# Kernel optimization log

Hardware: AMD Instinct MI355X
Metric: run time of the kernel (lower is better)

## Reference

```python
import jax, jax.numpy as jnp
import numpy as np

EPS = 1e-10   # eps added inside cumprod, as in _compute_weights
FAR = 1e10    # last delta, as in forward()
NEAR_D, FAR_D = 2.0, 6.0  # typical NeRF near/far bounds for depth sampling

N_RAYS, N_PTS = 65536, 128


def setup_inputs() -> dict:
    key = jax.random.key(0)
    k1, k2, k3 = jax.random.split(key, 3)
    # densities are non-negative (raw sigma output after relu/softplus)
    density = jax.random.uniform(k1, (N_RAYS, N_PTS), dtype=jnp.float32) * 2.0
    feature = jax.random.uniform(k2, (N_RAYS, N_PTS, 3), dtype=jnp.float32)
    # monotonically increasing sample depths along each ray in [NEAR_D, FAR_D]
    depth_values = jnp.sort(
        jax.random.uniform(k3, (N_RAYS, N_PTS), dtype=jnp.float32,
                           minval=NEAR_D, maxval=FAR_D), axis=-1)
    return {"density": density, "feature": feature, "depth_values": depth_values}


def reference(density, feature, depth_values):
    # deltas: diff of sample depths, last delta = 1e10  -> [N, P]
    deltas = jnp.concatenate(
        [depth_values[..., 1:] - depth_values[..., :-1],
         jnp.full_like(depth_values[..., :1], FAR)], axis=-1)
    alpha = 1.0 - jnp.exp(-deltas * density)                      # [N, P]
    # transmittance: cumprod(1-alpha+eps) rolled right with T[...,0]=1
    Tinc = jnp.cumprod(1.0 - alpha + EPS, axis=-1)                # [N, P]
    T = jnp.concatenate([jnp.ones_like(Tinc[..., :1]), Tinc[..., :-1]], axis=-1)
    weights = T * alpha                                           # [N, P]
    # weighted feature (rgb) and depth aggregation over samples
    rgb = jnp.einsum('np,npc->nc', weights, feature)              # [N, 3]
    depth = jnp.einsum('np,npc->nc', weights,
                       jnp.broadcast_to(depth_values[..., None], feature.shape))  # [N, 3]
    return rgb, depth
```

## Files before the change

### kernel.cpp

```cpp
#include <hip/hip_runtime.h>

#define N_PTS 128
#define EPS_F 1e-10f
#define FAR_F 1e10f
#define MAX_GRID 2048

template<int CTRL, int ROW_MASK>
__device__ __forceinline__ float dpp_mov(float src, float old) {
    union { float f; int i; } s, o, r;
    s.f = src; o.f = old;
    r.i = __builtin_amdgcn_update_dpp(o.i, s.i, CTRL, ROW_MASK, 0xF, false);
    return r.f;
}

__device__ __forceinline__ float half32_reduce_add(float x) {
    x += dpp_mov<0x111, 0xF>(x, 0.0f);
    x += dpp_mov<0x112, 0xF>(x, 0.0f);
    x += dpp_mov<0x114, 0xF>(x, 0.0f);
    x += dpp_mov<0x118, 0xF>(x, 0.0f);
    x += dpp_mov<0x142, 0xA>(x, 0.0f);
    return x;
}

__device__ __forceinline__ void process_pair(
        const float4& dns, const float4& zz,
        const float4& fa, const float4& fb, const float4& fc,
        int sub, int ray, int n_rays, float* __restrict__ out) {
    float nz = dpp_mov<0x130, 0xF>(zz.x, 0.0f);
    float d0 = zz.y - zz.x;
    float d1 = zz.z - zz.y;
    float d2 = zz.w - zz.z;
    float d3 = (sub == 31) ? FAR_F : (nz - zz.w);

    float e0 = __expf(-d0 * dns.x);
    float e1 = __expf(-d1 * dns.y);
    float e2 = __expf(-d2 * dns.z);
    float e3 = __expf(-d3 * dns.w);
    float a0 = 1.0f - e0, a1 = 1.0f - e1, a2 = 1.0f - e2, a3 = 1.0f - e3;
    float f0 = e0 + EPS_F, f1 = e1 + EPS_F, f2 = e2 + EPS_F, f3 = e3 + EPS_F;

    float f01  = f0 * f1;
    float f012 = f01 * f2;
    float p    = f012 * f3;
    p *= dpp_mov<0x111, 0xF>(p, 1.0f);
    p *= dpp_mov<0x112, 0xF>(p, 1.0f);
    p *= dpp_mov<0x114, 0xF>(p, 1.0f);
    p *= dpp_mov<0x118, 0xF>(p, 1.0f);
    p *= dpp_mov<0x142, 0xA>(p, 1.0f);
    float Ts = dpp_mov<0x138, 0xF>(p, 1.0f);
    if (sub == 0) Ts = 1.0f;

    float w0 = Ts * a0;
    float T1 = Ts * f0;   float w1 = T1 * a1;
    float T2 = Ts * f01;  float w2 = T2 * a2;
    float T3 = Ts * f012; float w3 = T3 * a3;

    float rx = half32_reduce_add(w0 * fa.x + w1 * fa.w + w2 * fb.z + w3 * fc.y);
    float ry = half32_reduce_add(w0 * fa.y + w1 * fb.x + w2 * fb.w + w3 * fc.z);
    float rz = half32_reduce_add(w0 * fa.z + w1 * fb.y + w2 * fc.x + w3 * fc.w);
    float dd = half32_reduce_add(w0 * zz.x + w1 * zz.y + w2 * zz.z + w3 * zz.w);

    if (sub == 31) {
        float* o  = out + (size_t)ray * 3;
        o[0] = rx; o[1] = ry; o[2] = rz;
        float* od = out + (size_t)n_rays * 3 + (size_t)ray * 3;
        od[0] = dd; od[1] = dd; od[2] = dd;
    }
}

__global__ __launch_bounds__(256) void volrend_kernel(
        const float* __restrict__ density,
        const float* __restrict__ feature,
        const float* __restrict__ depth,
        float* __restrict__ out, int n_rays, int iters) {
    const int lane = threadIdx.x & 63;
    const int sub  = lane & 31;
    const int h    = lane >> 5;
    const int gw   = blockIdx.x * 4 + (threadIdx.x >> 6);
    const int rstep = gridDim.x * 4 * 2;

    int ray0 = gw * 2 + h;
    size_t doff = (size_t)ray0 * N_PTS + (sub << 2);
    size_t foff = (size_t)ray0 * (N_PTS * 3) + sub * 12;
    const size_t dstep = (size_t)rstep * N_PTS;
    const size_t fstep = (size_t)rstep * (N_PTS * 3);

    float4 dA = *(const float4*)(density + doff);
    float4 zA = *(const float4*)(depth   + doff);
    const float4* fpA = (const float4*)(feature + foff);
    float4 aA = fpA[0], bA = fpA[1], cA = fpA[2];

    float4 dB, zB, aB, bB, cB;
    if (iters > 1) {
        dB = *(const float4*)(density + doff + dstep);
        zB = *(const float4*)(depth   + doff + dstep);
        const float4* fpB = (const float4*)(feature + foff + fstep);
        aB = fpB[0]; bB = fpB[1]; cB = fpB[2];
    }
    doff += 2 * dstep; foff += 2 * fstep;

    int ray_c = ray0;
    for (int k = 0; k < iters; k += 2) {
        process_pair(dA, zA, aA, bA, cA, sub, ray_c, n_rays, out);
        if (k + 2 < iters) {
            dA = *(const float4*)(density + doff);
            zA = *(const float4*)(depth   + doff);
            const float4* fp = (const float4*)(feature + foff);
            aA = fp[0]; bA = fp[1]; cA = fp[2];
            doff += dstep; foff += fstep;
        }
        ray_c += rstep;
        if (k + 1 >= iters) break;

        process_pair(dB, zB, aB, bB, cB, sub, ray_c, n_rays, out);
        if (k + 3 < iters) {
            dB = *(const float4*)(density + doff);
            zB = *(const float4*)(depth   + doff);
            const float4* fp = (const float4*)(feature + foff);
            aB = fp[0]; bB = fp[1]; cB = fp[2];
            doff += dstep; foff += fstep;
        }
        ray_c += rstep;
    }
}

extern "C" void kernel_launch(void* const* d_in, const int* in_sizes, int n_in,
                              void* d_out, int out_size, void* d_ws, size_t ws_size,
                              hipStream_t stream) {
    const float* density = (const float*)d_in[0];
    const float* feature = (const float*)d_in[1];
    const float* depth   = (const float*)d_in[2];
    float* out = (float*)d_out;
    const int n_rays = in_sizes[0] / N_PTS;
    int nblk8 = n_rays / 8;
    int grid = nblk8 < MAX_GRID ? nblk8 : MAX_GRID;
    while (grid > 1 && (nblk8 % grid)) --grid;
    const int iters = nblk8 / grid;
    volrend_kernel<<<grid, 256, 0, stream>>>(density, feature, depth, out,
                                             n_rays, iters);
}
```

Before: 192.4 us.

## Replace grid-stride double-buffered loop with one-ray-pair-per-wave launch and nontemporal loads

```diff
diff --git a/kernel.cpp b/kernel.cpp
--- a/kernel.cpp
+++ b/kernel.cpp
@@ -3,7 +3,8 @@
 #define N_PTS 128
 #define EPS_F 1e-10f
 #define FAR_F 1e10f
-#define MAX_GRID 2048
+
+typedef float f4 __attribute__((ext_vector_type(4)));
 
 template<int CTRL, int ROW_MASK>
 __device__ __forceinline__ float dpp_mov(float src, float old) {
@@ -22,10 +23,25 @@
     return x;
 }
 
-__device__ __forceinline__ void process_pair(
-        const float4& dns, const float4& zz,
-        const float4& fa, const float4& fb, const float4& fc,
-        int sub, int ray, int n_rays, float* __restrict__ out) {
+__global__ __launch_bounds__(256) void volrend_kernel(
+        const float* __restrict__ density,
+        const float* __restrict__ feature,
+        const float* __restrict__ depth,
+        float* __restrict__ out, int n_rays) {
+    const int lane = threadIdx.x & 63;
+    const int sub  = lane & 31;
+    const int h    = lane >> 5;
+    const int ray  = blockIdx.x * 8 + (threadIdx.x >> 6) * 2 + h;
+    if (ray >= n_rays) return;
+
+    const size_t doff = (size_t)ray * N_PTS + (sub << 2);
+    const f4 dns = __builtin_nontemporal_load((const f4*)(density + doff));
+    const f4 zz  = __builtin_nontemporal_load((const f4*)(depth   + doff));
+    const f4* fp = (const f4*)(feature + (size_t)ray * (N_PTS * 3) + sub * 12);
+    const f4 fa = __builtin_nontemporal_load(fp + 0);
+    const f4 fb = __builtin_nontemporal_load(fp + 1);
+    const f4 fc = __builtin_nontemporal_load(fp + 2);
+
     float nz = dpp_mov<0x130, 0xF>(zz.x, 0.0f);
     float d0 = zz.y - zz.x;
     float d1 = zz.z - zz.y;
@@ -68,62 +84,6 @@
     }
 }
 
-__global__ __launch_bounds__(256) void volrend_kernel(
-        const float* __restrict__ density,
-        const float* __restrict__ feature,
-        const float* __restrict__ depth,
-        float* __restrict__ out, int n_rays, int iters) {
-    const int lane = threadIdx.x & 63;
-    const int sub  = lane & 31;
-    const int h    = lane >> 5;
-    const int gw   = blockIdx.x * 4 + (threadIdx.x >> 6);
-    const int rstep = gridDim.x * 4 * 2;
-
-    int ray0 = gw * 2 + h;
-    size_t doff = (size_t)ray0 * N_PTS + (sub << 2);
-    size_t foff = (size_t)ray0 * (N_PTS * 3) + sub * 12;
-    const size_t dstep = (size_t)rstep * N_PTS;
-    const size_t fstep = (size_t)rstep * (N_PTS * 3);
-
-    float4 dA = *(const float4*)(density + doff);
-    float4 zA = *(const float4*)(depth   + doff);
-    const float4* fpA = (const float4*)(feature + foff);
-    float4 aA = fpA[0], bA = fpA[1], cA = fpA[2];
-
-    float4 dB, zB, aB, bB, cB;
-    if (iters > 1) {
-        dB = *(const float4*)(density + doff + dstep);
-        zB = *(const float4*)(depth   + doff + dstep);
-        const float4* fpB = (const float4*)(feature + foff + fstep);
-        aB = fpB[0]; bB = fpB[1]; cB = fpB[2];
-    }
-    doff += 2 * dstep; foff += 2 * fstep;
-
-    int ray_c = ray0;
-    for (int k = 0; k < iters; k += 2) {
-        process_pair(dA, zA, aA, bA, cA, sub, ray_c, n_rays, out);
-        if (k + 2 < iters) {
-            dA = *(const float4*)(density + doff);
-            zA = *(const float4*)(depth   + doff);
-            const float4* fp = (const float4*)(feature + foff);
-            aA = fp[0]; bA = fp[1]; cA = fp[2];
-            doff += dstep; foff += fstep;
-        }
-        ray_c += rstep;
-        if (k + 1 >= iters) break;
-
-        process_pair(dB, zB, aB, bB, cB, sub, ray_c, n_rays, out);
-        if (k + 3 < iters) {
-            dB = *(const float4*)(density + doff);
-            zB = *(const float4*)(depth   + doff);
-            const float4* fp = (const float4*)(feature + foff);
-            aB = fp[0]; bB = fp[1]; cB = fp[2];
-            doff += dstep; foff += fstep;
-        }
-        ray_c += rstep;
-    }
-}
-
 extern "C" void kernel_launch(void* const* d_in, const int* in_sizes, int n_in,
                               void* d_out, int out_size, void* d_ws, size_t ws_size,
                               hipStream_t stream) {
@@ -132,10 +92,6 @@
     const float* depth   = (const float*)d_in[2];
     float* out = (float*)d_out;
     const int n_rays = in_sizes[0] / N_PTS;
-    int nblk8 = n_rays / 8;
-    int grid = nblk8 < MAX_GRID ? nblk8 : MAX_GRID;
-    while (grid > 1 && (nblk8 % grid)) --grid;
-    const int iters = nblk8 / grid;
-    volrend_kernel<<<grid, 256, 0, stream>>>(density, feature, depth, out,
-                                             n_rays, iters);
+    const int blocks = (n_rays + 7) / 8;
+    volrend_kernel<<<blocks, 256, 0, stream>>>(density, feature, depth, out, n_rays);
 }
```

Measured after the change: 180.4 us, median of 2. 6.2% less time.
